# Kernel optimization log

Measured on AMD Instinct MI355X. Metric: run time of the kernel, lower is better.

## Reference

```python
import jax, jax.numpy as jnp
import numpy as np

B, T, D, H = 4, 2048, 1024, 4
DK = D // H      # head_k_dim = 256
DV = D // H      # head_v_dim = 256
M = DK           # num_slots defaults to head_k_dim
GATE_NORM = 16.0
CLAMP_MIN, CLAMP_MAX = -32.0, 32.0
EPS = 1e-5
ROPE_BASE = 10000.0


def setup_inputs() -> dict:
    key = jax.random.key(0)
    ks = jax.random.split(key, 8)
    sd = 0.02  # stands in for xavier_uniform with gain 2**-2.5
    return {
        "hidden_states": jax.random.normal(ks[0], (B, T, D), jnp.float32),
        "q_w": jax.random.normal(ks[1], (D, D), jnp.float32) * sd,
        "k_w": jax.random.normal(ks[2], (D, D), jnp.float32) * sd,
        "v_w": jax.random.normal(ks[3], (D, D), jnp.float32) * sd,
        "g_w": jax.random.normal(ks[4], (D, D), jnp.float32) * sd,
        "s_w": jax.random.normal(ks[5], (D, H * M), jnp.float32) * sd,
        "sg_w": jax.random.normal(ks[6], (D, H), jnp.float32) * sd,
        "gn_w": jnp.ones((DV,), jnp.float32),
        "o_w": jax.random.normal(ks[7], (D, D), jnp.float32) * sd,
    }


def _rope(x):
    # x: [B, T, H, DK]; non-interleaved (flash-attn style) rotary, full head dim
    half = x.shape[-1] // 2
    inv = 1.0 / (ROPE_BASE ** (jnp.arange(half, dtype=jnp.float32) / half))
    ang = jnp.arange(x.shape[1], dtype=jnp.float32)[:, None] * inv[None, :]  # [T, half]
    cos = jnp.cos(ang)[None, :, None, :]
    sin = jnp.sin(ang)[None, :, None, :]
    x1, x2 = x[..., :half], x[..., half:]
    return jnp.concatenate([x1 * cos - x2 * sin, x2 * cos + x1 * sin], -1)


def _abc(q, k, v, s):
    # ABC linear attention with slot memory (fla chunk_abc semantics, g=None path).
    # q, k: [B,H,T,DK]; v: [B,H,T,DV]; s: [B,H,T,M] (clamped slot logits)
    scale = q.shape[-1] ** -0.5
    z = jax.lax.cumlogsumexp(s, axis=2)                    # running log-normalizer
    s_n = jnp.exp(s - z)                                   # normalized slot write weights
    g = jnp.exp(jnp.concatenate([z[:, :, :1], z[:, :, :-1]], 2) - z)  # per-step decay in (0,1]

    tm = lambda x: jnp.moveaxis(x, 2, 0)                   # time-major for scan

    # stage 1: key memory  hk[B,H,DK,M];  ok_t = scale * q_t @ hk_t
    def step_k(hk, inp):
        q_t, k_t, s_t, g_t = inp
        hk = hk * g_t[:, :, None, :] + k_t[..., None] * s_t[:, :, None, :]
        return hk, jnp.einsum('bhk,bhkm->bhm', q_t, hk)
    hk0 = jnp.zeros(q.shape[:2] + (q.shape[-1], s.shape[-1]), q.dtype)
    _, ok = jax.lax.scan(step_k, hk0, (tm(q * scale), tm(k), tm(s_n), tm(g)))

    qv = jax.nn.softmax(ok, axis=-1)                       # slot read weights, [T,B,H,M]

    # stage 2: value memory  hv[B,H,M,DV];  ov_t = qv_t @ hv_t
    def step_v(hv, inp):
        qv_t, v_t, s_t, g_t = inp
        hv = hv * g_t[..., None] + s_t[..., None] * v_t[:, :, None, :]
        return hv, jnp.einsum('bhm,bhmv->bhv', qv_t, hv)
    hv0 = jnp.zeros(v.shape[:2] + (s.shape[-1], v.shape[-1]), v.dtype)
    _, ov = jax.lax.scan(step_v, hv0, (qv, tm(v), tm(s_n), tm(g)))
    return jnp.moveaxis(ov, 0, 2)                          # [B,H,T,DV]


def reference(hidden_states, q_w, k_w, v_w, g_w, s_w, sg_w, gn_w, o_w):
    x = hidden_states
    q = (x @ q_w).reshape(B, T, H, DK)
    k = (x @ k_w).reshape(B, T, H, DK)
    v = (x @ v_w).reshape(B, T, H, DV).transpose(0, 2, 1, 3)       # [B,H,T,DV]
    q, k = _rope(q), _rope(k)
    q = q.transpose(0, 2, 1, 3)                                    # [B,H,T,DK]
    k = k.transpose(0, 2, 1, 3)

    s = (x @ s_w).reshape(B, T, H, M).transpose(0, 2, 1, 3)        # [B,H,T,M]
    s = jnp.clip(s, CLAMP_MIN, CLAMP_MAX)

    sg = jax.nn.log_sigmoid(x @ sg_w).transpose(0, 2, 1) / GATE_NORM  # [B,H,T]
    k = k * jnp.exp(jnp.cumsum(sg, axis=2))[..., None]

    o = _abc(q, k, v, s).transpose(0, 2, 1, 3)                     # [B,T,H,DV]

    g = (x @ g_w).reshape(B, T, H, DV)
    rms = o * jax.lax.rsqrt(jnp.mean(o * o, axis=-1, keepdims=True) + EPS) * gn_w
    o = (rms * g * jax.nn.sigmoid(g)).reshape(B, T, D)             # RMSNorm + swish gate
    return o @ o_w
```

## Files before the change

### kernel.cpp

```cpp
#include <hip/hip_runtime.h>
#include <hip/hip_bf16.h>
#include <stdint.h>
#include <stddef.h>
#include <math.h>

typedef __bf16 bf8_t __attribute__((ext_vector_type(8)));
typedef __bf16 bf4_t __attribute__((ext_vector_type(4)));
typedef float  f4_t  __attribute__((ext_vector_type(4)));
typedef unsigned int u32;

#define DEV static __device__ __forceinline__

namespace abc {
constexpr int B = 4, T = 2048, D = 1024, H = 4;
constexpr int BT = B * T;
constexpr int CH = 64;
constexpr int NC = T / CH;
constexpr int BH = B * H;
constexpr float SCALE = 0.0625f;
constexpr float GN = 16.0f;
constexpr float EPS = 1e-5f;
}

DEV f4_t mfma16(bf8_t a, bf8_t b, f4_t c) {
  return __builtin_amdgcn_mfma_f32_16x16x32_bf16(a, b, c, 0, 0, 0);
}

DEV void glds16(const void* g, void* l) {
  __builtin_amdgcn_global_load_lds(
      (const __attribute__((address_space(1))) u32*)g,
      (__attribute__((address_space(3))) u32*)l, 16, 0, 0);
}

template<int ROWS>
DEV void stage(const __bf16* __restrict__ g, int S ,
               __bf16* lds, int tid) {
  #pragma unroll
  for (int i = 0; i < ROWS / 64; i++) {
    int p = i * 256 + tid;
    int m = p >> 2;
    int q = (p & 3) ^ (m & 3);
    glds16(g + (size_t)m * S + q * 8, lds + (i * 256 + (tid & ~63)) * 8);
  }
}
DEV bf8_t bfrag(const __bf16* sl, int m, int quad) {
  return *reinterpret_cast<const bf8_t*>(sl + m * 32 + ((quad ^ (m & 3)) << 3));
}

__global__ __launch_bounds__(256)
void cvt_x_kernel(const float* __restrict__ x, __bf16* __restrict__ xb)
{
  const int idx = blockIdx.x * 256 + threadIdx.x;
  const float4* src = reinterpret_cast<const float4*>(x);
  float4 a = src[(size_t)idx * 2];
  float4 b = src[(size_t)idx * 2 + 1];
  bf8_t o;
  o[0] = (__bf16)a.x; o[1] = (__bf16)a.y; o[2] = (__bf16)a.z; o[3] = (__bf16)a.w;
  o[4] = (__bf16)b.x; o[5] = (__bf16)b.y; o[6] = (__bf16)b.z; o[7] = (__bf16)b.w;
  reinterpret_cast<bf8_t*>(xb)[idx] = o;
}

__global__ __launch_bounds__(256)
void cvt_w_kernel(const float* __restrict__ w0, const float* __restrict__ w1,
                  const float* __restrict__ w2, const float* __restrict__ w3,
                  const float* __restrict__ w4, const float* __restrict__ w5,
                  __bf16* __restrict__ wt)
{
  const int z = blockIdx.z;
  const float* W = (z == 0) ? w0 : (z == 1) ? w1 : (z == 2) ? w2
                 : (z == 3) ? w3 : (z == 4) ? w4 : w5;
  const int n0 = blockIdx.x * 64, k0 = blockIdx.y * 64;
  __shared__ __bf16 Ts[64][72];
  const int tid = threadIdx.x;
  #pragma unroll
  for (int i = 0; i < 4; i++) {
    int p = tid + 256 * i;
    int row = p >> 4, c4 = p & 15;
    float4 v = *reinterpret_cast<const float4*>(W + (size_t)(k0 + row) * 1024 + n0 + c4 * 4);
    Ts[c4 * 4 + 0][row] = (__bf16)v.x;
    Ts[c4 * 4 + 1][row] = (__bf16)v.y;
    Ts[c4 * 4 + 2][row] = (__bf16)v.z;
    Ts[c4 * 4 + 3][row] = (__bf16)v.w;
  }
  __syncthreads();
  #pragma unroll
  for (int i = 0; i < 2; i++) {
    int p = tid + 256 * i;
    int n = p >> 3, kq = p & 7;
    bf8_t o = *reinterpret_cast<const bf8_t*>(&Ts[n][kq * 8]);
    *reinterpret_cast<bf8_t*>(wt + (size_t)z * 1024 * 1024 + (size_t)(n0 + n) * 1024 + k0 + kq * 8) = o;
  }
}

template<bool OUT_BF16, int NZ>
__global__ __launch_bounds__(256)
void gemm_bt_kernel(const __bf16* __restrict__ A, const __bf16* __restrict__ BtB,
                    void* __restrict__ Cp)
{
  using namespace abc;
  constexpr int K = 1024;
  constexpr int NZC = 8 * NZ;
  const int bflat = blockIdx.x;
  const int xcd = bflat & 7;
  const int j = bflat >> 3;
  const int m_local = j / NZC;
  const int nz = j % NZC;
  const int nt = nz & 7, z = nz >> 3;
  const int m0 = (xcd * 8 + m_local) * 128;
  const int n0 = nt * 128;
  const __bf16* Bt = BtB + (size_t)z * K * 1024;
  __shared__ __bf16 As[128 * 64];
  __shared__ __bf16 Bs[128 * 64];
  const int tid = threadIdx.x;
  const int lane = tid & 63, wvid = tid >> 6;
  const int wr = wvid >> 1, wc = wvid & 1;
  const int quad = lane >> 4, l16 = lane & 15;
  const f4_t fzero = {0.f, 0.f, 0.f, 0.f};
  f4_t acc[4][4];
  #pragma unroll
  for (int i = 0; i < 4; i++)
    #pragma unroll
    for (int j2 = 0; j2 < 4; j2++) acc[i][j2] = fzero;

  const int chunk_row = tid >> 3;
  const int chunk_col = tid & 7;
  for (int k0 = 0; k0 < K; k0 += 64) {
    __syncthreads();
    #pragma unroll
    for (int i = 0; i < 4; i++) {
      glds16(A + (size_t)(m0 + i * 32 + chunk_row) * K + k0 + chunk_col * 8,
             &As[(size_t)(i * 256 + wvid * 64) * 8]);
    }
    #pragma unroll
    for (int i = 0; i < 4; i++) {
      glds16(Bt + (size_t)(n0 + i * 32 + chunk_row) * K + k0 + chunk_col * 8,
             &Bs[(size_t)(i * 256 + wvid * 64) * 8]);
    }
    __syncthreads();
    #pragma unroll
    for (int ks = 0; ks < 2; ks++) {
      bf8_t af[4], bfv[4];
      #pragma unroll
      for (int i = 0; i < 4; i++)
        af[i] = *reinterpret_cast<const bf8_t*>(
            &As[(size_t)(wr * 64 + i * 16 + l16) * 64 + ks * 32 + quad * 8]);
      #pragma unroll
      for (int j2 = 0; j2 < 4; j2++)
        bfv[j2] = *reinterpret_cast<const bf8_t*>(
            &Bs[(size_t)(wc * 64 + j2 * 16 + l16) * 64 + ks * 32 + quad * 8]);
      #pragma unroll
      for (int i = 0; i < 4; i++)
        #pragma unroll
        for (int j2 = 0; j2 < 4; j2++)
          acc[i][j2] = mfma16(af[i], bfv[j2], acc[i][j2]);
    }
  }
  const int crow = m0 + wr * 64, ccol = n0 + wc * 64;
  if (OUT_BF16) {
    __bf16* C = (__bf16*)Cp + (size_t)z * BT * 1024;
    #pragma unroll
    for (int i = 0; i < 4; i++)
      #pragma unroll
      for (int j2 = 0; j2 < 4; j2++)
        #pragma unroll
        for (int r = 0; r < 4; r++)
          C[(size_t)(crow + i * 16 + quad * 4 + r) * 1024 + ccol + j2 * 16 + l16] =
              (__bf16)acc[i][j2][r];
  } else {
    float* C = (float*)Cp;
    #pragma unroll
    for (int i = 0; i < 4; i++)
      #pragma unroll
      for (int j2 = 0; j2 < 4; j2++)
        #pragma unroll
        for (int r = 0; r < 4; r++)
          C[(size_t)(crow + i * 16 + quad * 4 + r) * 1024 + ccol + j2 * 16 + l16] =
              acc[i][j2][r];
  }
}

__global__ __launch_bounds__(256)
void sg_kernel(const float* __restrict__ x, const float* __restrict__ sgw,
               float* __restrict__ sgl)
{
  using namespace abc;
  const int wvid = threadIdx.x >> 6, lane = threadIdx.x & 63;
  const int bt = blockIdx.x * 4 + wvid;
  const float* xr = x + (size_t)bt * 1024;
  float a0 = 0, a1 = 0, a2 = 0, a3 = 0;
  #pragma unroll 4
  for (int u = 0; u < 16; u++) {
    int i = u * 64 + lane;
    float xv = xr[i];
    float4 w = *reinterpret_cast<const float4*>(sgw + (size_t)i * 4);
    a0 += xv * w.x; a1 += xv * w.y; a2 += xv * w.z; a3 += xv * w.w;
  }
  #pragma unroll
  for (int off = 32; off > 0; off >>= 1) {
    a0 += __shfl_down(a0, off);
    a1 += __shfl_down(a1, off);
    a2 += __shfl_down(a2, off);
    a3 += __shfl_down(a3, off);
  }
  if (lane == 0) {
    const int b = bt >> 11, t = bt & (T - 1);
    float r[4] = {a0, a1, a2, a3};
    #pragma unroll
    for (int h = 0; h < 4; h++) {
      float v = r[h];
      float ls = fminf(v, 0.f) - log1pf(expf(-fabsf(v)));
      sgl[(size_t)(b * 4 + h) * T + t] = ls * (1.0f / GN);
    }
  }
}

__global__ __launch_bounds__(256)
void scan_kernel(const float* __restrict__ sgl, float* __restrict__ sgc)
{
  using namespace abc;
  const int bh = blockIdx.x;
  const float* in = sgl + (size_t)bh * T;
  float* out = sgc + (size_t)bh * T;
  __shared__ float part[256];
  const int tid = threadIdx.x;
  float v[8]; float s = 0.f;
  #pragma unroll
  for (int i = 0; i < 8; i++) { v[i] = in[tid * 8 + i]; s += v[i]; }
  part[tid] = s;
  __syncthreads();
  for (int off = 1; off < 256; off <<= 1) {
    float a = (tid >= off) ? part[tid - off] : 0.f;
    __syncthreads();
    part[tid] += a;
    __syncthreads();
  }
  float run = (tid > 0) ? part[tid - 1] : 0.f;
  #pragma unroll
  for (int i = 0; i < 8; i++) { run += v[i]; out[tid * 8 + i] = run; }
}

__global__ __launch_bounds__(256)
void prep_kernel(__bf16* __restrict__ q, __bf16* __restrict__ k,
                 __bf16* __restrict__ s, const float* __restrict__ sgc)
{
  using namespace abc;
  const int bt = blockIdx.x;
  const int b = bt >> 11, t = bt & (T - 1);
  const int tid = threadIdx.x;
  const size_t ro = (size_t)bt * 1024;
  #pragma unroll
  for (int i = 0; i < 2; i++) {
    int p = tid + 256 * i;
    int h = p >> 7, d = p & 127;
    float inv = expf(-(float)d * (9.210340371976184f / 128.0f));
    float ang = (float)t * inv;
    float sn, cs;
    sincosf(ang, &sn, &cs);
    size_t base = ro + (size_t)h * 256 + d;
    float q1 = (float)q[base], q2 = (float)q[base + 128];
    q[base]       = (__bf16)(q1 * cs - q2 * sn);
    q[base + 128] = (__bf16)(q2 * cs + q1 * sn);
    float dec = expf(sgc[(size_t)(b * 4 + h) * T + t]);
    float k1 = (float)k[base], k2 = (float)k[base + 128];
    k[base]       = (__bf16)((k1 * cs - k2 * sn) * dec);
    k[base + 128] = (__bf16)((k2 * cs + k1 * sn) * dec);
  }
  #pragma unroll
  for (int i = 0; i < 4; i++) {
    int e = tid + 256 * i;
    float v = (float)s[ro + e];
    v = fminf(fmaxf(v, -32.f), 32.f);
    s[ro + e] = (__bf16)expf(v);
  }
}

__global__ __launch_bounds__(256)
void transpose_kernel(const __bf16* __restrict__ s0, const __bf16* __restrict__ s1,
                      __bf16* __restrict__ d0, __bf16* __restrict__ d1)
{
  using namespace abc;
  const int c = blockIdx.x, bh = blockIdx.y, z = blockIdx.z;
  const int b = bh >> 2, h = bh & 3;
  const size_t R = (size_t)b * T + (size_t)c * CH;
  const int F = h * 256;
  const __bf16* src = z ? s1 : s0;
  __bf16* dst = (z ? d1 : d0) + ((size_t)bh * NC + c) * (256 * 64);
  __shared__ __bf16 L[256 * 64];
  const int tid = threadIdx.x;
  #pragma unroll
  for (int j = 0; j < 8; j++) {
    int p = tid + 256 * j;
    int t = p >> 5, fc = p & 31;
    bf8_t v = *reinterpret_cast<const bf8_t*>(src + (R + t) * 1024 + F + fc * 8);
    const int sw = ((t >> 3) ^ (fc & 7)) * 8 + (t & 7);
    #pragma unroll
    for (int u = 0; u < 8; u++)
      L[(fc * 8 + u) * 64 + sw] = v[u];
  }
  __syncthreads();
  #pragma unroll
  for (int j = 0; j < 8; j++) {
    int p = tid + 256 * j;
    int f = p >> 3, q = p & 7;
    int phys = q ^ ((f >> 3) & 7);
    bf8_t o = *reinterpret_cast<const bf8_t*>(&L[f * 64 + phys * 8]);
    *reinterpret_cast<bf8_t*>(dst + (size_t)f * 64 + q * 8) = o;
  }
}

__global__ __launch_bounds__(256)
void chunkstate_kernel(const __bf16* __restrict__ KT, const __bf16* __restrict__ VT,
                       const __bf16* __restrict__ AT,
                       __bf16* __restrict__ HKc, __bf16* __restrict__ HVc,
                       float* __restrict__ csA)
{
  using namespace abc;
  const int c = blockIdx.x, bh = blockIdx.y, part = blockIdx.z;
  const size_t TB = ((size_t)bh * NC + c) * (256 * 64);
  const bool isHV = part >= 2;
  const int p2 = part & 1;
  const __bf16* Aop = (isHV ? VT : AT) + TB;
  const __bf16* Bop = (isHV ? AT : KT) + TB;
  const int tid = threadIdx.x;
  if (part == 2) {
    float ssum = 0.f;
    #pragma unroll
    for (int u = 0; u < 8; u++) {
      bf8_t v = *reinterpret_cast<const bf8_t*>(AT + TB + (size_t)tid * 64 + u * 8);
      #pragma unroll
      for (int w = 0; w < 8; w++) ssum += (float)v[w];
    }
    csA[((size_t)bh * NC + c) * 256 + tid] = ssum;
  }
  const int lane = tid & 63, wvid = tid >> 6;
  const int quad = lane >> 4, l16 = lane & 15;
  const int row0 = p2 * 128 + wvid * 32;
  const f4_t fzero = {0.f, 0.f, 0.f, 0.f};
  f4_t acc[2][16];
  #pragma unroll
  for (int a = 0; a < 2; a++)
    #pragma unroll
    for (int ct = 0; ct < 16; ct++) acc[a][ct] = fzero;
  #pragma unroll
  for (int ks = 0; ks < 2; ks++) {
    bf8_t af0 = *reinterpret_cast<const bf8_t*>(Aop + (size_t)(row0 + l16) * 64 + ks * 32 + quad * 8);
    bf8_t af1 = *reinterpret_cast<const bf8_t*>(Aop + (size_t)(row0 + 16 + l16) * 64 + ks * 32 + quad * 8);
    #pragma unroll
    for (int ct = 0; ct < 16; ct++) {
      bf8_t bv = *reinterpret_cast<const bf8_t*>(Bop + (size_t)(ct * 16 + l16) * 64 + ks * 32 + quad * 8);
      acc[0][ct] = mfma16(af0, bv, acc[0][ct]);
      acc[1][ct] = mfma16(af1, bv, acc[1][ct]);
    }
  }
  __bf16* out = (isHV ? HVc : HKc) + ((size_t)bh * NC + c) * 65536;
  #pragma unroll
  for (int rt = 0; rt < 2; rt++)
    #pragma unroll
    for (int ct = 0; ct < 16; ct++)
      #pragma unroll
      for (int r = 0; r < 4; r++)
        out[(size_t)(row0 + rt * 16 + quad * 4 + r) * 256 + ct * 16 + l16] =
            (__bf16)acc[rt][ct][r];
}

__global__ __launch_bounds__(256)
void prefix_state_kernel(__bf16* __restrict__ HKc, __bf16* __restrict__ HVc)
{
  using namespace abc;
  const int bh = blockIdx.y;
  __bf16* base = (blockIdx.z ? HVc : HKc) + (size_t)bh * NC * 65536;
  const int e = (blockIdx.x * 256 + threadIdx.x) * 4;
  float run0 = 0, run1 = 0, run2 = 0, run3 = 0;
  for (int c = 0; c < NC; c++) {
    __bf16* p = base + (size_t)c * 65536 + e;
    bf4_t v = *reinterpret_cast<const bf4_t*>(p);
    bf4_t o;
    o[0] = (__bf16)run0; o[1] = (__bf16)run1; o[2] = (__bf16)run2; o[3] = (__bf16)run3;
    run0 += (float)v[0]; run1 += (float)v[1]; run2 += (float)v[2]; run3 += (float)v[3];
    *reinterpret_cast<bf4_t*>(p) = o;
  }
}

__global__ __launch_bounds__(256)
void prefix_csa_kernel(float* __restrict__ csA)
{
  using namespace abc;
  const int bh = blockIdx.x, m = threadIdx.x;
  float run = 0.f;
  for (int c = 0; c < NC; c++) {
    float* p = csA + ((size_t)bh * NC + c) * 256 + m;
    float v = *p; *p = run; run += v;
  }
}

__global__ __launch_bounds__(256)
void attn_kernel(const __bf16* __restrict__ qg, const __bf16* __restrict__ kg,
                 const __bf16* __restrict__ ag, const __bf16* __restrict__ gg,
                 const __bf16* __restrict__ ATp, const __bf16* __restrict__ VTp,
                 const __bf16* __restrict__ HKp, const __bf16* __restrict__ HVp,
                 const float* __restrict__ Zp, const float* __restrict__ gnw,
                 __bf16* __restrict__ yout)
{
  using namespace abc;
  const int c = blockIdx.x, bh = blockIdx.y;
  const int b = bh >> 2, h = bh & 3;
  const size_t R = (size_t)b * T + (size_t)c * CH;
  const int F = h * 256;
  const int tid = threadIdx.x;
  const int lane = tid & 63, wvid = tid >> 6;
  const int quad = lane >> 4, l16 = lane & 15;

  __shared__ __bf16 ST[2][8192];
  __shared__ __bf16 Ws[64][264];
  __shared__ __bf16 S1s[64][72];
  __shared__ float zs[256];
  __shared__ float gns[256];

  const __bf16* atb = ATp + ((size_t)bh * NC + c) * (256 * 64);
  const __bf16* vtb = VTp + ((size_t)bh * NC + c) * (256 * 64);
  const __bf16* hkb = HKp + ((size_t)bh * NC + c) * 65536;
  const __bf16* hvb = HVp + ((size_t)bh * NC + c) * 65536;
  const __bf16* kbase = kg + R * 1024 + F;
  const __bf16* abase = ag + R * 1024 + F;

  zs[tid] = Zp[((size_t)bh * NC + c) * 256 + tid];
  gns[tid] = gnw[tid];

  const __bf16* qrow = qg + (R + wvid * 16 + l16) * 1024 + F;
  bf8_t aq[8];
  #pragma unroll
  for (int ks = 0; ks < 8; ks++)
    aq[ks] = *reinterpret_cast<const bf8_t*>(qrow + ks * 32 + quad * 8);

  const f4_t fzero = {0.f, 0.f, 0.f, 0.f};

  stage<64>(kbase, 1024, ST[0], tid);
  __syncthreads();

  f4_t s1a[4];
  #pragma unroll
  for (int it = 0; it < 4; it++) s1a[it] = fzero;
  #pragma unroll
  for (int ks = 0; ks < 8; ks++) {
    if (ks < 7) stage<64>(kbase + (ks + 1) * 32, 1024, ST[(ks + 1) & 1], tid);
    else        stage<256>(atb, 64, ST[0], tid);
    const __bf16* sl = ST[ks & 1];
    #pragma unroll
    for (int it = 0; it < 4; it++) {
      bf8_t bk = bfrag(sl, it * 16 + l16, quad);
      s1a[it] = mfma16(aq[ks], bk, s1a[it]);
    }
    __syncthreads();
  }
  #pragma unroll
  for (int it = 0; it < 4; it++)
    #pragma unroll
    for (int r = 0; r < 4; r++) {
      int tl = wvid * 16 + quad * 4 + r;
      int il = it * 16 + l16;
      S1s[tl][il] = (il <= tl) ? (__bf16)s1a[it][r] : (__bf16)0.0f;
    }

  f4_t aok[16], acum[16];
  #pragma unroll
  for (int mt = 0; mt < 16; mt++) { aok[mt] = fzero; acum[mt] = fzero; }
  #pragma unroll
  for (int iks = 0; iks < 2; iks++) {
    if (iks == 0) stage<256>(atb + 32, 64, ST[1], tid);
    else          stage<256>(hkb, 256, ST[0], tid);
    const __bf16* sl = ST[iks & 1];
    bf8_t s1f = *reinterpret_cast<const bf8_t*>(&S1s[wvid * 16 + l16][iks * 32 + quad * 8]);
    bf8_t lf;
    #pragma unroll
    for (int j = 0; j < 8; j++)
      lf[j] = (iks * 32 + quad * 8 + j <= wvid * 16 + l16) ? (__bf16)1.0f : (__bf16)0.0f;
    #pragma unroll
    for (int mt = 0; mt < 16; mt++) {
      bf8_t bfa = bfrag(sl, mt * 16 + l16, quad);
      aok[mt]  = mfma16(s1f, bfa, aok[mt]);
      acum[mt] = mfma16(lf,  bfa, acum[mt]);
    }
    __syncthreads();
  }

  #pragma unroll
  for (int ks = 0; ks < 8; ks++) {
    if (ks < 7) stage<256>(hkb + (ks + 1) * 32, 256, ST[(ks + 1) & 1], tid);
    else        stage<64>(abase, 1024, ST[0], tid);
    const __bf16* sl = ST[ks & 1];
    #pragma unroll
    for (int mt = 0; mt < 16; mt++) {
      bf8_t bv = bfrag(sl, mt * 16 + l16, quad);
      aok[mt] = mfma16(aq[ks], bv, aok[mt]);
    }
    __syncthreads();
  }

  #pragma unroll
  for (int r = 0; r < 4; r++) {
    float ovv[16], sa[16];
    float mx = -3.0e38f;
    #pragma unroll
    for (int mt = 0; mt < 16; mt++) {
      sa[mt] = zs[mt * 16 + l16] + acum[mt][r];
      ovv[mt] = SCALE * aok[mt][r] / sa[mt];
      mx = fmaxf(mx, ovv[mt]);
    }
    #pragma unroll
    for (int off = 1; off < 16; off <<= 1) mx = fmaxf(mx, __shfl_xor(mx, off));
    float se = 0.f;
    #pragma unroll
    for (int mt = 0; mt < 16; mt++) { ovv[mt] = __expf(ovv[mt] - mx); se += ovv[mt]; }
    #pragma unroll
    for (int off = 1; off < 16; off <<= 1) se += __shfl_xor(se, off);
    float inv = 1.0f / se;
    int tl = wvid * 16 + quad * 4 + r;
    #pragma unroll
    for (int mt = 0; mt < 16; mt++)
      Ws[tl][mt * 16 + l16] = (__bf16)(ovv[mt] * inv / sa[mt]);
  }

  f4_t pacc[4];
  #pragma unroll
  for (int it = 0; it < 4; it++) pacc[it] = fzero;
  #pragma unroll
  for (int ks = 0; ks < 8; ks++) {
    if (ks < 7) stage<64>(abase + (ks + 1) * 32, 1024, ST[(ks + 1) & 1], tid);
    else        stage<256>(hvb, 256, ST[0], tid);
    const __bf16* sl = ST[ks & 1];
    bf8_t wf = *reinterpret_cast<const bf8_t*>(&Ws[wvid * 16 + l16][ks * 32 + quad * 8]);
    #pragma unroll
    for (int it = 0; it < 4; it++) {
      bf8_t ba = bfrag(sl, it * 16 + l16, quad);
      pacc[it] = mfma16(wf, ba, pacc[it]);
    }
    __syncthreads();
  }
  #pragma unroll
  for (int it = 0; it < 4; it++)
    #pragma unroll
    for (int r = 0; r < 4; r++) {
      int tl = wvid * 16 + quad * 4 + r;
      int il = it * 16 + l16;
      S1s[tl][il] = (il <= tl) ? (__bf16)pacc[it][r] : (__bf16)0.0f;
    }

  f4_t oacc[16];
  #pragma unroll
  for (int vt = 0; vt < 16; vt++) oacc[vt] = fzero;
  #pragma unroll
  for (int ks = 0; ks < 8; ks++) {
    if (ks < 7) stage<256>(hvb + (ks + 1) * 32, 256, ST[(ks + 1) & 1], tid);
    else        stage<256>(vtb, 64, ST[0], tid);
    const __bf16* sl = ST[ks & 1];
    bf8_t wf = *reinterpret_cast<const bf8_t*>(&Ws[wvid * 16 + l16][ks * 32 + quad * 8]);
    #pragma unroll
    for (int vt = 0; vt < 16; vt++) {
      bf8_t bv = bfrag(sl, vt * 16 + l16, quad);
      oacc[vt] = mfma16(wf, bv, oacc[vt]);
    }
    __syncthreads();
  }
  #pragma unroll
  for (int iks = 0; iks < 2; iks++) {
    if (iks == 0) stage<256>(vtb + 32, 64, ST[1], tid);
    const __bf16* sl = ST[iks & 1];
    bf8_t pf = *reinterpret_cast<const bf8_t*>(&S1s[wvid * 16 + l16][iks * 32 + quad * 8]);
    #pragma unroll
    for (int vt = 0; vt < 16; vt++) {
      bf8_t bvt = bfrag(sl, vt * 16 + l16, quad);
      oacc[vt] = mfma16(pf, bvt, oacc[vt]);
    }
    __syncthreads();
  }

  #pragma unroll
  for (int r = 0; r < 4; r++) {
    float ss = 0.f;
    #pragma unroll
    for (int vt = 0; vt < 16; vt++) ss += oacc[vt][r] * oacc[vt][r];
    #pragma unroll
    for (int off = 1; off < 16; off <<= 1) ss += __shfl_xor(ss, off);
    float rinv = rsqrtf(ss * (1.0f / 256.0f) + EPS);
    int tl = wvid * 16 + quad * 4 + r;
    const __bf16* grow = gg + (R + tl) * 1024 + F;
    __bf16* yrow = yout + (R + tl) * 1024 + F;
    #pragma unroll
    for (int vt = 0; vt < 16; vt++) {
      int v = vt * 16 + l16;
      float gvl = (float)grow[v];
      float yv = oacc[vt][r] * rinv * gns[v] * gvl / (1.0f + __expf(-gvl));
      yrow[v] = (__bf16)yv;
    }
  }
}

extern "C" void kernel_launch(void* const* d_in, const int* in_sizes, int n_in,
                              void* d_out, int out_size, void* d_ws, size_t ws_size,
                              hipStream_t stream) {
  using namespace abc;
  (void)in_sizes; (void)n_in; (void)out_size; (void)ws_size;
  const float* x    = (const float*)d_in[0];
  const float* q_w  = (const float*)d_in[1];
  const float* k_w  = (const float*)d_in[2];
  const float* v_w  = (const float*)d_in[3];
  const float* g_w  = (const float*)d_in[4];
  const float* s_w  = (const float*)d_in[5];
  const float* sg_w = (const float*)d_in[6];
  const float* gn_w = (const float*)d_in[7];
  const float* o_w  = (const float*)d_in[8];
  float* out = (float*)d_out;

  char* ws = (char*)d_ws;
  const size_t PROJ = (size_t)BT * 1024;
  __bf16* proj = (__bf16*)ws;
  __bf16* q_bf = proj + 0 * PROJ;
  __bf16* k_bf = proj + 1 * PROJ;
  __bf16* v_bf = proj + 2 * PROJ;
  __bf16* g_bf = proj + 3 * PROJ;
  __bf16* a_bf = proj + 4 * PROJ;
  __bf16* xb   = proj + 5 * PROJ;
  float* sgl = (float*)(ws + (size_t)96 * 1024 * 1024);
  float* sgc = sgl + (size_t)BH * T;
  float* csA = sgc + (size_t)BH * T;
  __bf16* HKc = (__bf16*)(ws + (size_t)97 * 1024 * 1024);
  __bf16* HVc = HKc + (size_t)BH * NC * 65536;
  __bf16* wt  = (__bf16*)(ws + (size_t)225 * 1024 * 1024);
  __bf16* KT  = (__bf16*)(ws + (size_t)237 * 1024 * 1024);
  __bf16* VT  = xb;
  __bf16* AT  = v_bf;
  __bf16* y_bf = KT;

  dim3 blk(256);
  cvt_w_kernel<<<dim3(16, 16, 6), blk, 0, stream>>>(q_w, k_w, v_w, g_w, s_w, o_w, wt);
  cvt_x_kernel<<<dim3(BT * 1024 / (256 * 8)), blk, 0, stream>>>(x, xb);
  gemm_bt_kernel<true, 5><<<dim3(64 * 8 * 5), blk, 0, stream>>>(xb, wt, proj);
  sg_kernel<<<dim3(BT / 4), blk, 0, stream>>>(x, sg_w, sgl);
  scan_kernel<<<dim3(BH), blk, 0, stream>>>(sgl, sgc);
  prep_kernel<<<dim3(BT), blk, 0, stream>>>(q_bf, k_bf, a_bf, sgc);
  transpose_kernel<<<dim3(NC, BH, 2), blk, 0, stream>>>(k_bf, v_bf, KT, VT);
  transpose_kernel<<<dim3(NC, BH, 1), blk, 0, stream>>>(a_bf, a_bf, AT, AT);
  chunkstate_kernel<<<dim3(NC, BH, 4), blk, 0, stream>>>(KT, VT, AT, HKc, HVc, csA);
  prefix_state_kernel<<<dim3(64, BH, 2), blk, 0, stream>>>(HKc, HVc);
  prefix_csa_kernel<<<dim3(BH), blk, 0, stream>>>(csA);
  attn_kernel<<<dim3(NC, BH), blk, 0, stream>>>(
      q_bf, k_bf, a_bf, g_bf, AT, VT, HKc, HVc, csA, gn_w, y_bf);
  gemm_bt_kernel<false, 1><<<dim3(64 * 8), blk, 0, stream>>>(
      y_bf, wt + (size_t)5 * 1024 * 1024, out);
}
```

Baseline: 497.0 us.

## Pipeline attn kernel loads through a 4-slot LDS ring with manual waitcnts

Replaces the attention kernel's double-buffered staging, which ended every step with a full __syncthreads, with a unified 48-stage schedule over a 4-slot LDS ring. Loads are issued three stages ahead and each stage waits only on the vmcnt it needs, so more global-to-LDS transfers overlap with MFMA work. The prefix_state kernel is also widened to 8 elements per thread with a partially unrolled loop and half the blocks. Hand-written waitcnt counts are fragile: they assume a fixed number of outstanding loads per stage, and getting them wrong would silently read stale LDS data.

```diff
diff --git a/kernel.cpp b/kernel.cpp
--- a/kernel.cpp
+++ b/kernel.cpp
@@ -45,6 +45,14 @@
 }
 DEV bf8_t bfrag(const __bf16* sl, int m, int quad) {
   return *reinterpret_cast<const bf8_t*>(sl + m * 32 + ((quad ^ (m & 3)) << 3));
+}
+
+DEV void ring_pre(int s) {
+  if (s < 46)       asm volatile("s_waitcnt vmcnt(4)" ::: "memory");
+  else if (s == 46) asm volatile("s_waitcnt vmcnt(2)" ::: "memory");
+  else              asm volatile("s_waitcnt vmcnt(0)" ::: "memory");
+  asm volatile("s_waitcnt lgkmcnt(0)" ::: "memory");
+  asm volatile("s_barrier" ::: "memory");
 }
 
 __global__ __launch_bounds__(256)
@@ -369,15 +377,18 @@
   using namespace abc;
   const int bh = blockIdx.y;
   __bf16* base = (blockIdx.z ? HVc : HKc) + (size_t)bh * NC * 65536;
-  const int e = (blockIdx.x * 256 + threadIdx.x) * 4;
-  float run0 = 0, run1 = 0, run2 = 0, run3 = 0;
+  const int e = (blockIdx.x * 256 + threadIdx.x) * 8;
+  float run[8];
+  #pragma unroll
+  for (int u = 0; u < 8; u++) run[u] = 0.f;
+  #pragma unroll 4
   for (int c = 0; c < NC; c++) {
     __bf16* p = base + (size_t)c * 65536 + e;
-    bf4_t v = *reinterpret_cast<const bf4_t*>(p);
-    bf4_t o;
-    o[0] = (__bf16)run0; o[1] = (__bf16)run1; o[2] = (__bf16)run2; o[3] = (__bf16)run3;
-    run0 += (float)v[0]; run1 += (float)v[1]; run2 += (float)v[2]; run3 += (float)v[3];
-    *reinterpret_cast<bf4_t*>(p) = o;
+    bf8_t v = *reinterpret_cast<const bf8_t*>(p);
+    bf8_t o;
+    #pragma unroll
+    for (int u = 0; u < 8; u++) { o[u] = (__bf16)run[u]; run[u] += (float)v[u]; }
+    *reinterpret_cast<bf8_t*>(p) = o;
   }
 }
 
@@ -410,7 +421,7 @@
   const int lane = tid & 63, wvid = tid >> 6;
   const int quad = lane >> 4, l16 = lane & 15;
 
-  __shared__ __bf16 ST[2][8192];
+  __shared__ __bf16 ST[4][4096];
   __shared__ __bf16 Ws[64][264];
   __shared__ __bf16 S1s[64][72];
   __shared__ float zs[256];
@@ -425,6 +436,7 @@
 
   zs[tid] = Zp[((size_t)bh * NC + c) * 256 + tid];
   gns[tid] = gnw[tid];
+  __syncthreads();
 
   const __bf16* qrow = qg + (R + wvid * 16 + l16) * 1024 + F;
   bf8_t aq[8];
@@ -434,23 +446,49 @@
 
   const f4_t fzero = {0.f, 0.f, 0.f, 0.f};
 
-  stage<64>(kbase, 1024, ST[0], tid);
-  __syncthreads();
+  auto issue = [&](int s) {
+    if (s >= 48) return;
+    __bf16* buf = &ST[s & 3][0];
+    if (s < 4) {
+      stage<64>(kbase + (2 * s) * 32, 1024, buf, tid);
+      stage<64>(kbase + (2 * s + 1) * 32, 1024, buf + 2048, tid);
+    } else if (s < 8) {
+      int j = s - 4, iks = j >> 1, rh = j & 1;
+      stage<128>(atb + rh * 128 * 64 + iks * 32, 64, buf, tid);
+    } else if (s < 24) {
+      int j = s - 8, ks = j >> 1, rh = j & 1;
+      stage<128>(hkb + (size_t)rh * 128 * 256 + ks * 32, 256, buf, tid);
+    } else if (s < 28) {
+      int j = s - 24;
+      stage<64>(abase + (2 * j) * 32, 1024, buf, tid);
+      stage<64>(abase + (2 * j + 1) * 32, 1024, buf + 2048, tid);
+    } else if (s < 44) {
+      int j = s - 28, ks = j >> 1, rh = j & 1;
+      stage<128>(hvb + (size_t)rh * 128 * 256 + ks * 32, 256, buf, tid);
+    } else {
+      int j = s - 44, iks = j >> 1, rh = j & 1;
+      stage<128>(vtb + rh * 128 * 64 + iks * 32, 64, buf, tid);
+    }
+  };
+
+  issue(0); issue(1); issue(2);
 
   f4_t s1a[4];
   #pragma unroll
   for (int it = 0; it < 4; it++) s1a[it] = fzero;
   #pragma unroll
-  for (int ks = 0; ks < 8; ks++) {
-    if (ks < 7) stage<64>(kbase + (ks + 1) * 32, 1024, ST[(ks + 1) & 1], tid);
-    else        stage<256>(atb, 64, ST[0], tid);
-    const __bf16* sl = ST[ks & 1];
-    #pragma unroll
-    for (int it = 0; it < 4; it++) {
-      bf8_t bk = bfrag(sl, it * 16 + l16, quad);
-      s1a[it] = mfma16(aq[ks], bk, s1a[it]);
-    }
-    __syncthreads();
+  for (int j = 0; j < 4; j++) {
+    ring_pre(j);
+    issue(j + 3);
+    const __bf16* sl = &ST[j & 3][0];
+    #pragma unroll
+    for (int ks2 = 0; ks2 < 2; ks2++) {
+      bf8_t a = aq[2 * j + ks2];
+      const __bf16* sb = sl + ks2 * 2048;
+      #pragma unroll
+      for (int it = 0; it < 4; it++)
+        s1a[it] = mfma16(a, bfrag(sb, it * 16 + l16, quad), s1a[it]);
+    }
   }
   #pragma unroll
   for (int it = 0; it < 4; it++)
@@ -465,35 +503,35 @@
   #pragma unroll
   for (int mt = 0; mt < 16; mt++) { aok[mt] = fzero; acum[mt] = fzero; }
   #pragma unroll
-  for (int iks = 0; iks < 2; iks++) {
-    if (iks == 0) stage<256>(atb + 32, 64, ST[1], tid);
-    else          stage<256>(hkb, 256, ST[0], tid);
-    const __bf16* sl = ST[iks & 1];
+  for (int j = 0; j < 4; j++) {
+    int s = 4 + j, iks = j >> 1, rh = j & 1;
+    ring_pre(s);
+    issue(s + 3);
+    const __bf16* sl = &ST[s & 3][0];
     bf8_t s1f = *reinterpret_cast<const bf8_t*>(&S1s[wvid * 16 + l16][iks * 32 + quad * 8]);
     bf8_t lf;
     #pragma unroll
-    for (int j = 0; j < 8; j++)
-      lf[j] = (iks * 32 + quad * 8 + j <= wvid * 16 + l16) ? (__bf16)1.0f : (__bf16)0.0f;
-    #pragma unroll
-    for (int mt = 0; mt < 16; mt++) {
-      bf8_t bfa = bfrag(sl, mt * 16 + l16, quad);
-      aok[mt]  = mfma16(s1f, bfa, aok[mt]);
-      acum[mt] = mfma16(lf,  bfa, acum[mt]);
-    }
-    __syncthreads();
-  }
-
-  #pragma unroll
-  for (int ks = 0; ks < 8; ks++) {
-    if (ks < 7) stage<256>(hkb + (ks + 1) * 32, 256, ST[(ks + 1) & 1], tid);
-    else        stage<64>(abase, 1024, ST[0], tid);
-    const __bf16* sl = ST[ks & 1];
-    #pragma unroll
-    for (int mt = 0; mt < 16; mt++) {
-      bf8_t bv = bfrag(sl, mt * 16 + l16, quad);
-      aok[mt] = mfma16(aq[ks], bv, aok[mt]);
-    }
-    __syncthreads();
+    for (int u = 0; u < 8; u++)
+      lf[u] = (iks * 32 + quad * 8 + u <= wvid * 16 + l16) ? (__bf16)1.0f : (__bf16)0.0f;
+    #pragma unroll
+    for (int m8 = 0; m8 < 8; m8++) {
+      bf8_t bfa = bfrag(sl, m8 * 16 + l16, quad);
+      aok[rh * 8 + m8]  = mfma16(s1f, bfa, aok[rh * 8 + m8]);
+      acum[rh * 8 + m8] = mfma16(lf,  bfa, acum[rh * 8 + m8]);
+    }
+  }
+
+  #pragma unroll
+  for (int j = 0; j < 16; j++) {
+    int s = 8 + j, ks = j >> 1, rh = j & 1;
+    ring_pre(s);
+    issue(s + 3);
+    const __bf16* sl = &ST[s & 3][0];
+    #pragma unroll
+    for (int m8 = 0; m8 < 8; m8++) {
+      bf8_t bv = bfrag(sl, m8 * 16 + l16, quad);
+      aok[rh * 8 + m8] = mfma16(aq[ks], bv, aok[rh * 8 + m8]);
+    }
   }
 
   #pragma unroll
@@ -524,17 +562,20 @@
   #pragma unroll
   for (int it = 0; it < 4; it++) pacc[it] = fzero;
   #pragma unroll
-  for (int ks = 0; ks < 8; ks++) {
-    if (ks < 7) stage<64>(abase + (ks + 1) * 32, 1024, ST[(ks + 1) & 1], tid);
-    else        stage<256>(hvb, 256, ST[0], tid);
-    const __bf16* sl = ST[ks & 1];
-    bf8_t wf = *reinterpret_cast<const bf8_t*>(&Ws[wvid * 16 + l16][ks * 32 + quad * 8]);
-    #pragma unroll
-    for (int it = 0; it < 4; it++) {
-      bf8_t ba = bfrag(sl, it * 16 + l16, quad);
-      pacc[it] = mfma16(wf, ba, pacc[it]);
-    }
-    __syncthreads();
+  for (int j = 0; j < 4; j++) {
+    int s = 24 + j;
+    ring_pre(s);
+    issue(s + 3);
+    const __bf16* sl = &ST[s & 3][0];
+    #pragma unroll
+    for (int ks2 = 0; ks2 < 2; ks2++) {
+      int ks = 2 * j + ks2;
+      bf8_t wf = *reinterpret_cast<const bf8_t*>(&Ws[wvid * 16 + l16][ks * 32 + quad * 8]);
+      const __bf16* sb = sl + ks2 * 2048;
+      #pragma unroll
+      for (int it = 0; it < 4; it++)
+        pacc[it] = mfma16(wf, bfrag(sb, it * 16 + l16, quad), pacc[it]);
+    }
   }
   #pragma unroll
   for (int it = 0; it < 4; it++)
@@ -549,29 +590,31 @@
   #pragma unroll
   for (int vt = 0; vt < 16; vt++) oacc[vt] = fzero;
   #pragma unroll
-  for (int ks = 0; ks < 8; ks++) {
-    if (ks < 7) stage<256>(hvb + (ks + 1) * 32, 256, ST[(ks + 1) & 1], tid);
-    else        stage<256>(vtb, 64, ST[0], tid);
-    const __bf16* sl = ST[ks & 1];
+  for (int j = 0; j < 16; j++) {
+    int s = 28 + j, ks = j >> 1, rh = j & 1;
+    ring_pre(s);
+    issue(s + 3);
+    const __bf16* sl = &ST[s & 3][0];
     bf8_t wf = *reinterpret_cast<const bf8_t*>(&Ws[wvid * 16 + l16][ks * 32 + quad * 8]);
     #pragma unroll
-    for (int vt = 0; vt < 16; vt++) {
-      bf8_t bv = bfrag(sl, vt * 16 + l16, quad);
-      oacc[vt] = mfma16(wf, bv, oacc[vt]);
-    }
-    __syncthreads();
-  }
-  #pragma unroll
-  for (int iks = 0; iks < 2; iks++) {
-    if (iks == 0) stage<256>(vtb + 32, 64, ST[1], tid);
-    const __bf16* sl = ST[iks & 1];
+    for (int v8 = 0; v8 < 8; v8++) {
+      bf8_t bv = bfrag(sl, v8 * 16 + l16, quad);
+      oacc[rh * 8 + v8] = mfma16(wf, bv, oacc[rh * 8 + v8]);
+    }
+  }
+
+  #pragma unroll
+  for (int j = 0; j < 4; j++) {
+    int s = 44 + j, iks = j >> 1, rh = j & 1;
+    ring_pre(s);
+    issue(s + 3);
+    const __bf16* sl = &ST[s & 3][0];
     bf8_t pf = *reinterpret_cast<const bf8_t*>(&S1s[wvid * 16 + l16][iks * 32 + quad * 8]);
     #pragma unroll
-    for (int vt = 0; vt < 16; vt++) {
-      bf8_t bvt = bfrag(sl, vt * 16 + l16, quad);
-      oacc[vt] = mfma16(pf, bvt, oacc[vt]);
-    }
-    __syncthreads();
+    for (int v8 = 0; v8 < 8; v8++) {
+      bf8_t bvt = bfrag(sl, v8 * 16 + l16, quad);
+      oacc[rh * 8 + v8] = mfma16(pf, bvt, oacc[rh * 8 + v8]);
+    }
   }
 
   #pragma unroll
@@ -641,7 +684,7 @@
   transpose_kernel<<<dim3(NC, BH, 2), blk, 0, stream>>>(k_bf, v_bf, KT, VT);
   transpose_kernel<<<dim3(NC, BH, 1), blk, 0, stream>>>(a_bf, a_bf, AT, AT);
   chunkstate_kernel<<<dim3(NC, BH, 4), blk, 0, stream>>>(KT, VT, AT, HKc, HVc, csA);
-  prefix_state_kernel<<<dim3(64, BH, 2), blk, 0, stream>>>(HKc, HVc);
+  prefix_state_kernel<<<dim3(32, BH, 2), blk, 0, stream>>>(HKc, HVc);
   prefix_csa_kernel<<<dim3(BH), blk, 0, stream>>>(csA);
   attn_kernel<<<dim3(NC, BH), blk, 0, stream>>>(
       q_bf, k_bf, a_bf, g_bf, AT, VT, HKc, HVc, csA, gn_w, y_bf);
```

Result: slower. 513.4 us (+3.3%).
